# Kernel tuning notes

Hardware: AMD Instinct MI355X
Metric: run time of the kernel (lower is better)

The kernel has to match this reference:

```python
import jax, jax.numpy as jnp
import numpy as np

T = 256        # number of time steps (len(ts))
B = 4096       # batch of independent ODE trajectories
D = 64         # data_size (state dim)
W = 256        # width_size
DT = 0.01      # time step


def setup_inputs() -> dict:
    key = jax.random.key(0)
    ks = jax.random.split(key, 9)
    ts = jnp.arange(T, dtype=jnp.float32) * DT
    y0 = jax.random.normal(ks[0], (B, D), dtype=jnp.float32)
    # MLP params: layers D->W, W->W, W->W, W->D (depth=3 hidden layers)
    def lin(k, out_d, in_d):
        return jax.random.normal(k, (out_d, in_d), dtype=jnp.float32) / np.float32(np.sqrt(in_d))
    w0 = lin(ks[1], W, D)
    b0 = jax.random.normal(ks[2], (W,), dtype=jnp.float32) * 0.01
    w1 = lin(ks[3], W, W)
    b1 = jax.random.normal(ks[4], (W,), dtype=jnp.float32) * 0.01
    w2 = lin(ks[5], W, W)
    b2 = jax.random.normal(ks[6], (W,), dtype=jnp.float32) * 0.01
    w3 = lin(ks[7], D, W)
    b3 = jax.random.normal(ks[8], (D,), dtype=jnp.float32) * 0.01
    return {"ts": ts, "y0": y0, "w0": w0, "b0": b0, "w1": w1, "b1": b1,
            "w2": w2, "b2": b2, "w3": w3, "b3": b3}


def reference(ts, y0, w0, b0, w1, b1, w2, b2, w3, b3):
    def mlp(y):  # y: [B, D] -> [B, D], softplus hidden activations
        h = jax.nn.softplus(y @ w0.T + b0)
        h = jax.nn.softplus(h @ w1.T + b1)
        h = jax.nn.softplus(h @ w2.T + b2)
        return h @ w3.T + b3

    dt = ts[1] - ts[0]

    def step(y, _):
        k1 = mlp(y)
        # NOTE: faithful to source: perturbations are 0.5*k1 and 0.75*k2 (no dt factor)
        k2 = mlp(y + 0.5 * k1)
        k3 = mlp(y + 0.75 * k2)
        y1 = (2.0 / 9.0 * k1 + 1.0 / 3.0 * k2 + 4.0 / 9.0 * k3) * dt + y
        return y1, y1

    _, ys = jax.lax.scan(step, y0, xs=None, length=ts.shape[0])
    return ys  # [T, B, D]
```

## Files before the change

### kernel.cpp

```cpp
#include <hip/hip_runtime.h>
#include <stdint.h>
#include <stddef.h>

constexpr int T_STEPS  = 256;
constexpr int B_ROWS   = 4096;
constexpr int D_DIM    = 64;
constexpr int W_DIM    = 256;
constexpr int ROWS_PB  = 16;
constexpr int NTHREADS = 512;

constexpr int HS_LD = 132;
constexpr int YB_LD = 36;

constexpr float LOG2E = 1.44269504088896f;
constexpr float LN2   = 0.693147180559945f;

typedef __attribute__((ext_vector_type(8))) __bf16 bf16x8;
typedef __attribute__((ext_vector_type(8))) short  short8;
typedef __attribute__((ext_vector_type(4))) float  f32x4;

__device__ __forceinline__ unsigned f2bf_bits(float f) {
    union { float f; unsigned u; } v; v.f = f;
    return (v.u + 0x7FFFu + ((v.u >> 16) & 1u)) >> 16;
}

__device__ __forceinline__ uint32_t cvt_pk_bf16(float lo, float hi) {
    uint32_t r;
    asm("v_cvt_pk_bf16_f32 %0, %1, %2" : "=v"(r) : "v"(lo), "v"(hi));
    return r;
}

__device__ __forceinline__ float act_g(float u) {
    float e = __builtin_amdgcn_exp2f(-fabsf(u));
    return fmaxf(u, 0.0f) + __builtin_amdgcn_logf(1.0f + e);
}

__device__ __forceinline__ bf16x8 load_wfrag(const float* __restrict__ wg, int ldk,
                                             int f, int kcb, int lg, float scale) {
    const float4 a = *reinterpret_cast<const float4*>(wg + (size_t)f * ldk + kcb + lg * 4);
    const float4 b = *reinterpret_cast<const float4*>(wg + (size_t)f * ldk + kcb + 16 + lg * 4);
    short8 s;
    s[0] = (short)f2bf_bits(a.x * scale); s[1] = (short)f2bf_bits(b.x * scale);
    s[2] = (short)f2bf_bits(a.y * scale); s[3] = (short)f2bf_bits(b.y * scale);
    s[4] = (short)f2bf_bits(a.z * scale); s[5] = (short)f2bf_bits(b.z * scale);
    s[6] = (short)f2bf_bits(a.w * scale); s[7] = (short)f2bf_bits(b.w * scale);
    return __builtin_bit_cast(bf16x8, s);
}

template<int NKC>
__device__ __forceinline__ void mlp_layer(const uint32_t* __restrict__ src,
                                          uint32_t* __restrict__ dst,
                                          const bf16x8* wf0, const bf16x8* wf1,
                                          float b0v, float b1v)
{
    f32x4 a0 = {b0v, b0v, b0v, b0v};
    f32x4 a1 = {b1v, b1v, b1v, b1v};
#pragma unroll
    for (int kc = 0; kc < NKC; ++kc) {
        const bf16x8 a = *reinterpret_cast<const bf16x8*>(src + kc * 16);
        a0 = __builtin_amdgcn_mfma_f32_16x16x32_bf16(a, wf0[kc], a0, 0, 0, 0);
        a1 = __builtin_amdgcn_mfma_f32_16x16x32_bf16(a, wf1[kc], a1, 0, 0, 0);
    }
#pragma unroll
    for (int j = 0; j < 4; ++j)
        dst[j * HS_LD] = cvt_pk_bf16(act_g(a0[j]), act_g(a1[j]));
}

__global__ __launch_bounds__(NTHREADS, 2) void node_rk3_kernel(
    const float* __restrict__ ts,
    const float* __restrict__ y0,
    const float* __restrict__ w0, const float* __restrict__ b0,
    const float* __restrict__ w1, const float* __restrict__ b1,
    const float* __restrict__ w2, const float* __restrict__ b2,
    const float* __restrict__ w3, const float* __restrict__ b3,
    float* __restrict__ out)
{
    __shared__ __align__(16) uint32_t hs0[ROWS_PB][HS_LD];
    __shared__ __align__(16) uint32_t hs1[ROWS_PB][HS_LD];
    __shared__ __align__(16) uint32_t ybf[ROWS_PB][YB_LD];

    const int tid  = threadIdx.x;
    const int lane = tid & 63;
    const int wid  = tid >> 6;
    const int lr   = lane & 15;
    const int lg   = lane >> 4;
    const int row0 = blockIdx.x * ROWS_PB;
    const int fbdw = wid * 16;

    bf16x8 w0f[2][2], w1f[2][8], w2f[2][8], w3f[8];
#pragma unroll
    for (int nt = 0; nt < 2; ++nt) {
        const int f = wid * 32 + nt * 16 + lr;
#pragma unroll
        for (int kc = 0; kc < 2; ++kc) w0f[nt][kc] = load_wfrag(w0, D_DIM, f, kc * 32, lg, LOG2E);
#pragma unroll
        for (int kc = 0; kc < 8; ++kc) w1f[nt][kc] = load_wfrag(w1, W_DIM, f, kc * 32, lg, 1.0f);
#pragma unroll
        for (int kc = 0; kc < 8; ++kc) w2f[nt][kc] = load_wfrag(w2, W_DIM, f, kc * 32, lg, 1.0f);
    }
    const int f3 = (wid & 3) * 16;
#pragma unroll
    for (int kc = 0; kc < 8; ++kc) w3f[kc] = load_wfrag(w3, W_DIM, f3 + lr, kc * 32, lg, LN2);

    const float bA0 = LOG2E * b0[wid * 32 + lr], bB0 = LOG2E * b0[wid * 32 + 16 + lr];
    const float bA1 = LOG2E * b1[wid * 32 + lr], bB1 = LOG2E * b1[wid * 32 + 16 + lr];
    const float bA2 = LOG2E * b2[wid * 32 + lr], bB2 = LOG2E * b2[wid * 32 + 16 + lr];
    const float bv3 = b3[f3 + lr];

    const float dt = ts[1] - ts[0];

    const uint32_t* pA_y  = &ybf[lr][lg * 4];
    const uint32_t* pA_h0 = &hs0[lr][lg * 4];
    const uint32_t* pA_h1 = &hs1[lr][lg * 4];
    uint32_t* pW_h0 = &hs0[lg * 4][fbdw + lr];
    uint32_t* pW_h1 = &hs1[lg * 4][fbdw + lr];
    const int kb = wid >> 1, hi = wid & 1;
    uint16_t* pYW = (uint16_t*)&ybf[0][0] + ((size_t)(lg * 4) * YB_LD + kb * 16 + lr) * 2 + hi;

    float yreg[4], k1r[4], k2r[4], vst[4];
#pragma unroll
    for (int j = 0; j < 4; ++j) {
        yreg[j] = y0[(size_t)(row0 + lg * 4 + j) * D_DIM + f3 + lr];
        k1r[j] = 0.f; k2r[j] = 0.f; vst[j] = 0.f;
    }

    for (int i = tid; i < ROWS_PB * 32; i += NTHREADS) {
        const int r = i >> 5, c32 = i & 31, kbi = c32 >> 4, u = c32 & 15;
        const float* yr = y0 + (size_t)(row0 + r) * D_DIM;
        ybf[r][kbi * 16 + u] = cvt_pk_bf16(yr[kbi * 32 + u], yr[kbi * 32 + 16 + u]);
    }
    __syncthreads();

    for (int t = 0; t < T_STEPS; ++t) {
        if (wid < 4 && t > 0) {
#pragma unroll
            for (int j = 0; j < 4; ++j)
                out[((size_t)(t - 1) * B_ROWS + row0 + lg * 4 + j) * D_DIM + f3 + lr] = vst[j];
        }
#pragma unroll
        for (int c = 0; c < 3; ++c) {
            mlp_layer<2>(pA_y,  pW_h0, w0f[0], w0f[1], bA0, bB0);
            __syncthreads();
            mlp_layer<8>(pA_h0, pW_h1, w1f[0], w1f[1], bA1, bB1);
            __syncthreads();
            mlp_layer<8>(pA_h1, pW_h0, w2f[0], w2f[1], bA2, bB2);
            __syncthreads();
            if (wid < 4) {
                f32x4 acc = {bv3, bv3, bv3, bv3};
#pragma unroll
                for (int kc = 0; kc < 8; ++kc) {
                    const bf16x8 a = *reinterpret_cast<const bf16x8*>(pA_h0 + kc * 16);
                    acc = __builtin_amdgcn_mfma_f32_16x16x32_bf16(a, w3f[kc], acc, 0, 0, 0);
                }
#pragma unroll
                for (int j = 0; j < 4; ++j) {
                    float v;
                    if (c == 0)      { k1r[j] = acc[j]; v = fmaf(0.5f,  acc[j], yreg[j]); }
                    else if (c == 1) { k2r[j] = acc[j]; v = fmaf(0.75f, acc[j], yreg[j]); }
                    else {
                        v = yreg[j] + dt * ((2.0f / 9.0f) * k1r[j]
                                          + (1.0f / 3.0f) * k2r[j]
                                          + (4.0f / 9.0f) * acc[j]);
                        yreg[j] = v;
                        vst[j]  = v;
                    }
                    pYW[j * YB_LD * 2] = (uint16_t)cvt_pk_bf16(v, v);
                }
            }
            __syncthreads();
        }
    }
    if (wid < 4) {
#pragma unroll
        for (int j = 0; j < 4; ++j)
            out[((size_t)(T_STEPS - 1) * B_ROWS + row0 + lg * 4 + j) * D_DIM + f3 + lr] = vst[j];
    }
}

extern "C" void kernel_launch(void* const* d_in, const int* in_sizes, int n_in,
                              void* d_out, int out_size, void* d_ws, size_t ws_size,
                              hipStream_t stream) {
    const float* ts = (const float*)d_in[0];
    const float* y0 = (const float*)d_in[1];
    const float* w0 = (const float*)d_in[2];
    const float* b0 = (const float*)d_in[3];
    const float* w1 = (const float*)d_in[4];
    const float* b1 = (const float*)d_in[5];
    const float* w2 = (const float*)d_in[6];
    const float* b2 = (const float*)d_in[7];
    const float* w3 = (const float*)d_in[8];
    const float* b3 = (const float*)d_in[9];
    float* out = (float*)d_out;

    hipLaunchKernelGGL(node_rk3_kernel,
                       dim3(B_ROWS / ROWS_PB), dim3(NTHREADS), 0, stream,
                       ts, y0, w0, b0, w1, b1, w2, b2, w3, b3, out);
}
```

Baseline: 1.399 ms.

## Halve block to four waves, each computing 64 hidden features per layer

Cuts the block from 8 to 4 waves. Each wave now holds weight fragments for 64 hidden features and runs four independent MFMA accumulator chains per layer. In the final layer all four waves now do useful work, where before half the waves sat idle, and fewer waves take part in each barrier. The trade-off is double the per-wave weight registers, which risks spills, and only one wave per SIMD to hide latency.

```diff
diff --git a/kernel.cpp b/kernel.cpp
--- a/kernel.cpp
+++ b/kernel.cpp
@@ -7,7 +7,7 @@
 constexpr int D_DIM    = 64;
 constexpr int W_DIM    = 256;
 constexpr int ROWS_PB  = 16;
-constexpr int NTHREADS = 512;
+constexpr int NTHREADS = 256;
 
 constexpr int HS_LD = 132;
 constexpr int YB_LD = 36;
@@ -48,25 +48,34 @@
 }
 
 template<int NKC>
-__device__ __forceinline__ void mlp_layer(const uint32_t* __restrict__ src,
-                                          uint32_t* __restrict__ dst,
-                                          const bf16x8* wf0, const bf16x8* wf1,
-                                          float b0v, float b1v)
+__device__ __forceinline__ void mlp_layer4(const uint32_t* __restrict__ src,
+                                           uint32_t* __restrict__ dst,
+                                           const bf16x8* __restrict__ wf0,
+                                           const bf16x8* __restrict__ wf1,
+                                           const bf16x8* __restrict__ wf2,
+                                           const bf16x8* __restrict__ wf3,
+                                           float bv0, float bv1, float bv2, float bv3)
 {
-    f32x4 a0 = {b0v, b0v, b0v, b0v};
-    f32x4 a1 = {b1v, b1v, b1v, b1v};
+    f32x4 a0 = {bv0, bv0, bv0, bv0};
+    f32x4 a1 = {bv1, bv1, bv1, bv1};
+    f32x4 a2 = {bv2, bv2, bv2, bv2};
+    f32x4 a3 = {bv3, bv3, bv3, bv3};
 #pragma unroll
     for (int kc = 0; kc < NKC; ++kc) {
         const bf16x8 a = *reinterpret_cast<const bf16x8*>(src + kc * 16);
         a0 = __builtin_amdgcn_mfma_f32_16x16x32_bf16(a, wf0[kc], a0, 0, 0, 0);
         a1 = __builtin_amdgcn_mfma_f32_16x16x32_bf16(a, wf1[kc], a1, 0, 0, 0);
-    }
-#pragma unroll
-    for (int j = 0; j < 4; ++j)
-        dst[j * HS_LD] = cvt_pk_bf16(act_g(a0[j]), act_g(a1[j]));
-}
-
-__global__ __launch_bounds__(NTHREADS, 2) void node_rk3_kernel(
+        a2 = __builtin_amdgcn_mfma_f32_16x16x32_bf16(a, wf2[kc], a2, 0, 0, 0);
+        a3 = __builtin_amdgcn_mfma_f32_16x16x32_bf16(a, wf3[kc], a3, 0, 0, 0);
+    }
+#pragma unroll
+    for (int j = 0; j < 4; ++j) {
+        dst[j * HS_LD]      = cvt_pk_bf16(act_g(a0[j]), act_g(a1[j]));
+        dst[j * HS_LD + 16] = cvt_pk_bf16(act_g(a2[j]), act_g(a3[j]));
+    }
+}
+
+__global__ __launch_bounds__(NTHREADS, 1) void node_rk3_kernel(
     const float* __restrict__ ts,
     const float* __restrict__ y0,
     const float* __restrict__ w0, const float* __restrict__ b0,
@@ -85,12 +94,11 @@
     const int lr   = lane & 15;
     const int lg   = lane >> 4;
     const int row0 = blockIdx.x * ROWS_PB;
-    const int fbdw = wid * 16;
-
-    bf16x8 w0f[2][2], w1f[2][8], w2f[2][8], w3f[8];
-#pragma unroll
-    for (int nt = 0; nt < 2; ++nt) {
-        const int f = wid * 32 + nt * 16 + lr;
+
+    bf16x8 w0f[4][2], w1f[4][8], w2f[4][8], w3f[8];
+#pragma unroll
+    for (int nt = 0; nt < 4; ++nt) {
+        const int f = wid * 64 + nt * 16 + lr;
 #pragma unroll
         for (int kc = 0; kc < 2; ++kc) w0f[nt][kc] = load_wfrag(w0, D_DIM, f, kc * 32, lg, LOG2E);
 #pragma unroll
@@ -98,13 +106,17 @@
 #pragma unroll
         for (int kc = 0; kc < 8; ++kc) w2f[nt][kc] = load_wfrag(w2, W_DIM, f, kc * 32, lg, 1.0f);
     }
-    const int f3 = (wid & 3) * 16;
+    const int f3 = wid * 16;
 #pragma unroll
     for (int kc = 0; kc < 8; ++kc) w3f[kc] = load_wfrag(w3, W_DIM, f3 + lr, kc * 32, lg, LN2);
 
-    const float bA0 = LOG2E * b0[wid * 32 + lr], bB0 = LOG2E * b0[wid * 32 + 16 + lr];
-    const float bA1 = LOG2E * b1[wid * 32 + lr], bB1 = LOG2E * b1[wid * 32 + 16 + lr];
-    const float bA2 = LOG2E * b2[wid * 32 + lr], bB2 = LOG2E * b2[wid * 32 + 16 + lr];
+    float bA0[4], bA1[4], bA2[4];
+#pragma unroll
+    for (int nt = 0; nt < 4; ++nt) {
+        bA0[nt] = LOG2E * b0[wid * 64 + nt * 16 + lr];
+        bA1[nt] = LOG2E * b1[wid * 64 + nt * 16 + lr];
+        bA2[nt] = LOG2E * b2[wid * 64 + nt * 16 + lr];
+    }
     const float bv3 = b3[f3 + lr];
 
     const float dt = ts[1] - ts[0];
@@ -112,8 +124,8 @@
     const uint32_t* pA_y  = &ybf[lr][lg * 4];
     const uint32_t* pA_h0 = &hs0[lr][lg * 4];
     const uint32_t* pA_h1 = &hs1[lr][lg * 4];
-    uint32_t* pW_h0 = &hs0[lg * 4][fbdw + lr];
-    uint32_t* pW_h1 = &hs1[lg * 4][fbdw + lr];
+    uint32_t* pW_h0 = &hs0[lg * 4][wid * 32 + lr];
+    uint32_t* pW_h1 = &hs1[lg * 4][wid * 32 + lr];
     const int kb = wid >> 1, hi = wid & 1;
     uint16_t* pYW = (uint16_t*)&ybf[0][0] + ((size_t)(lg * 4) * YB_LD + kb * 16 + lr) * 2 + hi;
 
@@ -132,20 +144,23 @@
     __syncthreads();
 
     for (int t = 0; t < T_STEPS; ++t) {
-        if (wid < 4 && t > 0) {
+        if (t > 0) {
 #pragma unroll
             for (int j = 0; j < 4; ++j)
                 out[((size_t)(t - 1) * B_ROWS + row0 + lg * 4 + j) * D_DIM + f3 + lr] = vst[j];
         }
 #pragma unroll
         for (int c = 0; c < 3; ++c) {
-            mlp_layer<2>(pA_y,  pW_h0, w0f[0], w0f[1], bA0, bB0);
-            __syncthreads();
-            mlp_layer<8>(pA_h0, pW_h1, w1f[0], w1f[1], bA1, bB1);
-            __syncthreads();
-            mlp_layer<8>(pA_h1, pW_h0, w2f[0], w2f[1], bA2, bB2);
-            __syncthreads();
-            if (wid < 4) {
+            mlp_layer4<2>(pA_y,  pW_h0, w0f[0], w0f[1], w0f[2], w0f[3],
+                          bA0[0], bA0[1], bA0[2], bA0[3]);
+            __syncthreads();
+            mlp_layer4<8>(pA_h0, pW_h1, w1f[0], w1f[1], w1f[2], w1f[3],
+                          bA1[0], bA1[1], bA1[2], bA1[3]);
+            __syncthreads();
+            mlp_layer4<8>(pA_h1, pW_h0, w2f[0], w2f[1], w2f[2], w2f[3],
+                          bA2[0], bA2[1], bA2[2], bA2[3]);
+            __syncthreads();
+            {
                 f32x4 acc = {bv3, bv3, bv3, bv3};
 #pragma unroll
                 for (int kc = 0; kc < 8; ++kc) {
@@ -170,11 +185,9 @@
             __syncthreads();
         }
     }
-    if (wid < 4) {
-#pragma unroll
-        for (int j = 0; j < 4; ++j)
-            out[((size_t)(T_STEPS - 1) * B_ROWS + row0 + lg * 4 + j) * D_DIM + f3 + lr] = vst[j];
-    }
+#pragma unroll
+    for (int j = 0; j < 4; ++j)
+        out[((size_t)(T_STEPS - 1) * B_ROWS + row0 + lg * 4 + j) * D_DIM + f3 + lr] = vst[j];
 }
 
 extern "C" void kernel_launch(void* const* d_in, const int* in_sizes, int n_in,
```

Result: slower. 1.867 ms (+33.5%).
